# Optimization experiments

Hardware: AMD Instinct MI355X
Metric: run time of the kernel (lower is better)

## Reference

```python
import jax, jax.numpy as jnp
import numpy as np

N_NODES = 100000
N_EDGES = 6400000
IN_CH = 128
HID = 32
OUT = 16


def setup_inputs() -> dict:
    key = jax.random.key(0)
    k1, k2, k3, k4 = jax.random.split(key, 4)
    x = jax.random.normal(k1, (N_NODES, IN_CH), dtype=jnp.float32)
    edge_index = jax.random.randint(k2, (2, N_EDGES), 0, N_NODES, dtype=jnp.int64)
    # Glorot-style init like PyG GCNConv
    W1 = jax.random.normal(k3, (IN_CH, HID), dtype=jnp.float32) * (1.0 / np.sqrt(IN_CH))
    b1 = jnp.zeros((HID,), dtype=jnp.float32)
    W2 = jax.random.normal(k4, (HID, OUT), dtype=jnp.float32) * (1.0 / np.sqrt(HID))
    b2 = jnp.zeros((OUT,), dtype=jnp.float32)
    return {"x": x, "edge_index": edge_index, "W1": W1, "b1": b1, "W2": W2, "b2": b2}


def _gcn_layer(h, W, b, row, col, norm, n_nodes):
    # transform then propagate (PyG GCNConv order)
    m = h @ W                                   # [N, F_out]
    msg = m[row] * norm[:, None]                # gather + scale, [E+N, F_out]
    agg = jax.ops.segment_sum(msg, col, num_segments=n_nodes)
    return agg + b


def reference(x, edge_index, W1, b1, W2, b2):
    n = x.shape[0]
    loops = jnp.arange(n, dtype=edge_index.dtype)
    row = jnp.concatenate([edge_index[0], loops])  # source
    col = jnp.concatenate([edge_index[1], loops])  # target (aggregation index)
    # symmetric GCN normalization with self-loops; deg >= 1 always
    deg = jax.ops.segment_sum(jnp.ones_like(col, dtype=x.dtype), col, num_segments=n)
    deg_inv_sqrt = jax.lax.rsqrt(deg)
    norm = deg_inv_sqrt[row] * deg_inv_sqrt[col]
    h = jax.nn.relu(_gcn_layer(x, W1, b1, row, col, norm, n))
    # dropout p=0.5 is identity in eval mode
    return _gcn_layer(h, W2, b2, row, col, norm, n)
```

## Files before the change

kernel.cpp:

```cpp
#include <hip/hip_runtime.h>
#include <hip/hip_bf16.h>

#define IN_CH 128
#define HID 32
#define OUT_CH 16
#define NPW 128
#define NPW_SHIFT 7
#define NB_MAX 1024
#define CAPF 12800
#define FBT 512
#define CAP 12288
#define KEYS (NPW * 2)
#define SCAN_CHUNK 1024
#define NXCD 8
#define EPT 8

typedef int vint4 __attribute__((ext_vector_type(4)));
typedef vint4 vint4u __attribute__((aligned(4)));
typedef float vfloat2 __attribute__((ext_vector_type(2)));

__global__ void detect_dtype(const void* ei, long long ecount, int n, int* flag) {
    int lane = threadIdx.x;
    const long long* p = (const long long*)ei;
    long long st = ecount / 64; if (st < 1) st = 1;
    long long idx = (long long)lane * st;
    bool ok = true;
    if (idx < ecount) {
        long long v = p[idx];
        ok = (v >= 0 && v < n);
    }
    unsigned long long mask = __ballot(ok);
    if (lane == 0) *flag = (mask == ~0ULL) ? 1 : 0;
}

__device__ __forceinline__ int load_idx(const void* ei, long long i, int is64) {
    return is64 ? (int)((const long long*)ei)[i] : ((const int*)ei)[i];
}

__device__ __forceinline__ void load_idx8_nt(const void* ei, long long off, int is64,
                                             int* c) {
    if (is64) {
        const long long* p = (const long long*)ei + off;
#pragma unroll
        for (int j = 0; j < 8; ++j) c[j] = (int)__builtin_nontemporal_load(p + j);
    } else {
        vint4 v0 = __builtin_nontemporal_load((const vint4*)((const int*)ei + off));
        vint4 v1 = __builtin_nontemporal_load((const vint4*)((const int*)ei + off + 4));
        c[0] = v0.x; c[1] = v0.y; c[2] = v0.z; c[3] = v0.w;
        c[4] = v1.x; c[5] = v1.y; c[6] = v1.z; c[7] = v1.w;
    }
}

__device__ __forceinline__ float bf_lo(unsigned int u) { return __uint_as_float(u << 16); }
__device__ __forceinline__ float bf_hi(unsigned int u) { return __uint_as_float(u & 0xFFFF0000u); }

__global__ __launch_bounds__(256) void zero_int(int* p, int n) {
    int i = blockIdx.x * 256 + threadIdx.x;
    if (i < n) p[i] = 0;
}

__global__ __launch_bounds__(256) void zero_float(float* p, long long n) {
    long long i = (long long)blockIdx.x * 256 + threadIdx.x;
    if (i < n) p[i] = 0.f;
}

__global__ __launch_bounds__(FBT) void bucket_hist(const void* ei, long long E,
                                                   const int* flag, int* bhist,
                                                   int nb, long long chunk, int fbgrid) {
    __shared__ int hist[NB_MAX];
    for (int i = threadIdx.x; i < nb; i += FBT) hist[i] = 0;
    __syncthreads();
    long long lo = (long long)blockIdx.x * chunk;
    long long hi = lo + chunk; if (hi > E) hi = E;
    int is64 = *flag;
    if ((E & 7) == 0) {
        for (long long e = lo + (long long)threadIdx.x * EPT; e + EPT <= hi;
             e += (long long)FBT * EPT) {
            int c[8]; load_idx8_nt(ei, E + e, is64, c);
#pragma unroll
            for (int j = 0; j < 8; ++j) atomicAdd(&hist[c[j] >> NPW_SHIFT], 1);
        }
    } else {
        for (long long e = lo + threadIdx.x; e < hi; e += FBT)
            atomicAdd(&hist[load_idx(ei, E + e, is64) >> NPW_SHIFT], 1);
    }
    __syncthreads();
    for (int b = threadIdx.x; b < nb; b += FBT)
        bhist[(long long)b * fbgrid + blockIdx.x] = hist[b];
}

__global__ __launch_bounds__(256) void scan_blocks(const int* bhist, int* bexcl,
                                                   int* btot, int nb, int fbgrid) {
    __shared__ int sd[256];
    int b = blockIdx.x, t = threadIdx.x;
    const int* p = bhist + (long long)b * fbgrid;
    int* q = bexcl + (long long)b * fbgrid;
    int running = 0;
    for (int j0 = 0; j0 < fbgrid; j0 += 256) {
        int j = j0 + t;
        int v = (j < fbgrid) ? p[j] : 0;
        sd[t] = v; __syncthreads();
        for (int off = 1; off < 256; off <<= 1) {
            int u = (t >= off) ? sd[t - off] : 0;
            __syncthreads(); sd[t] += u; __syncthreads();
        }
        if (j < fbgrid) q[j] = running + sd[t] - v;
        int tot = sd[255];
        __syncthreads();
        running += tot;
    }
    if (t == 0) btot[b] = running;
}

__global__ __launch_bounds__(1024) void scan_buckets(const int* btot, int* bstart, int nb) {
    __shared__ int sd[1024];
    int t = threadIdx.x;
    int a0 = (2 * t < nb) ? btot[2 * t] : 0;
    int a1 = (2 * t + 1 < nb) ? btot[2 * t + 1] : 0;
    sd[t] = a0 + a1; __syncthreads();
    for (int off = 1; off < 1024; off <<= 1) {
        int v = (t >= off) ? sd[t - off] : 0;
        __syncthreads(); sd[t] += v; __syncthreads();
    }
    int excl = sd[t] - (a0 + a1);
    if (2 * t < nb)     bstart[2 * t] = excl;
    if (2 * t + 1 < nb) bstart[2 * t + 1] = excl + a0;
    if (t == 1023) bstart[nb] = sd[t];
}

__global__ __launch_bounds__(FBT) void fill_sort(const void* ei, long long E,
                                                 const int* flag, const int* bhist,
                                                 const int* bexcl, const int* bstart,
                                                 int* bucketed, int nb,
                                                 long long chunk, int fbgrid) {
    __shared__ int lds[CAPF];
    __shared__ int hist[NB_MAX];
    __shared__ int base[NB_MAX];
    __shared__ int cur[NB_MAX];
    int blk = blockIdx.x, t = threadIdx.x;
    long long lo = (long long)blk * chunk;
    long long hi = lo + chunk; if (hi > E) hi = E;
    int cnt = (int)(hi - lo);
    for (int b = t; b < nb; b += FBT)
        hist[b] = bhist[(long long)b * fbgrid + blk];
    __syncthreads();
    int is64 = *flag;
    bool vec = ((E & 7) == 0) && ((chunk & 7) == 0);

    if (cnt <= CAPF) {
        int a0 = (2 * t < nb) ? hist[2 * t] : 0;
        int a1 = (2 * t + 1 < nb) ? hist[2 * t + 1] : 0;
        base[t] = a0 + a1; __syncthreads();
        for (int off = 1; off < FBT; off <<= 1) {
            int u = (t >= off) ? base[t - off] : 0;
            __syncthreads(); base[t] += u; __syncthreads();
        }
        int incl = base[t];
        __syncthreads();
        int excl = incl - (a0 + a1);
        if (2 * t < nb)     { base[2 * t] = excl;          cur[2 * t] = excl; }
        if (2 * t + 1 < nb) { base[2 * t + 1] = excl + a0; cur[2 * t + 1] = excl + a0; }
        __syncthreads();

        if (vec) {
            for (long long e = lo + (long long)t * EPT; e + EPT <= hi; e += (long long)FBT * EPT) {
                int c[8], r[8];
                load_idx8_nt(ei, E + e, is64, c);
                load_idx8_nt(ei, e, is64, r);
#pragma unroll
                for (int j = 0; j < 8; ++j) {
                    int b = c[j] >> NPW_SHIFT;
                    int p = atomicAdd(&cur[b], 1);
                    lds[p] = r[j] | ((c[j] & (NPW - 1)) << 17);
                }
            }
        } else {
            for (long long e = lo + t; e < hi; e += FBT) {
                int col = load_idx(ei, E + e, is64);
                int row = load_idx(ei, e, is64);
                int b = col >> NPW_SHIFT;
                int p = atomicAdd(&cur[b], 1);
                lds[p] = row | ((col & (NPW - 1)) << 17);
            }
        }
        __syncthreads();

        int grp = t >> 4, lane = t & 15;
        for (int b = grp; b < nb; b += 32) {
            int l0 = base[b], c0 = hist[b];
            if (!c0) continue;
            int g0 = bstart[b] + bexcl[(long long)b * fbgrid + blk];
            for (int j = lane; j < c0; j += 16)
                bucketed[g0 + j] = lds[l0 + j];
        }
    } else {
        for (int b = t; b < nb; b += FBT)
            cur[b] = bstart[b] + bexcl[(long long)b * fbgrid + blk];
        __syncthreads();
        for (long long e = lo + t; e < hi; e += FBT) {
            int col = load_idx(ei, E + e, is64);
            int row = load_idx(ei, e, is64);
            int b = col >> NPW_SHIFT;
            int p = atomicAdd(&cur[b], 1);
            bucketed[p] = row | ((col & (NPW - 1)) << 17);
        }
    }
}

__global__ __launch_bounds__(512) void csr_sort(const int* __restrict__ bucketed,
                                                const int* __restrict__ bstart,
                                                int* __restrict__ csr,
                                                int* __restrict__ offs,
                                                int* __restrict__ mid,
                                                float* __restrict__ dinv,
                                                int nb, int n, int nhalf) {
    __shared__ int lds_e[CAP];
    __shared__ int histk[KEYS];
    __shared__ int cur[KEYS];
    int b = blockIdx.x, t = threadIdx.x;
    int s0 = bstart[b], s1 = bstart[b + 1];
    int cnt = s1 - s0;
    if (t < KEYS) histk[t] = 0;
    __syncthreads();
    bool fit = (cnt <= CAP);
    int cnt4 = cnt & ~3;
    auto key = [&](int e) {
        return (((e >> 17) & (NPW - 1)) << 1) | (((e & 0x1FFFF) >= nhalf) ? 1 : 0);
    };
    if (fit) {
        for (int i = t * 4; i < cnt4; i += 2048) {
            vint4u e4 = *(const vint4u*)(bucketed + s0 + i);
            lds_e[i + 0] = e4.x; atomicAdd(&histk[key(e4.x)], 1);
            lds_e[i + 1] = e4.y; atomicAdd(&histk[key(e4.y)], 1);
            lds_e[i + 2] = e4.z; atomicAdd(&histk[key(e4.z)], 1);
            lds_e[i + 3] = e4.w; atomicAdd(&histk[key(e4.w)], 1);
        }
        for (int i = cnt4 + t; i < cnt; i += 512) {
            int e = bucketed[s0 + i];
            lds_e[i] = e;
            atomicAdd(&histk[key(e)], 1);
        }
    } else {
        for (int i = t * 4; i < cnt4; i += 2048) {
            vint4u e4 = *(const vint4u*)(bucketed + s0 + i);
            atomicAdd(&histk[key(e4.x)], 1);
            atomicAdd(&histk[key(e4.y)], 1);
            atomicAdd(&histk[key(e4.z)], 1);
            atomicAdd(&histk[key(e4.w)], 1);
        }
        for (int i = cnt4 + t; i < cnt; i += 512)
            atomicAdd(&histk[key(bucketed[s0 + i])], 1);
    }
    __syncthreads();
    if (t == 0) {
        int run = 0;
        for (int k = 0; k < KEYS; ++k) { cur[k] = run; run += histk[k]; }
    }
    __syncthreads();
    if (t < NPW) {
        int node = b * NPW + t;
        if (node < n) {
            offs[node] = s0 + cur[2 * t];
            mid[node]  = s0 + cur[2 * t] + histk[2 * t];
            dinv[node] = 1.0f / sqrtf((float)(histk[2 * t] + histk[2 * t + 1] + 1));
        }
    }
    if (b == nb - 1 && t == 0) offs[n] = s1;
    __syncthreads();
    if (fit) {
        for (int i = t; i < cnt; i += 512) {
            int e = lds_e[i];
            int pos = atomicAdd(&cur[key(e)], 1);
            csr[s0 + pos] = e & 0x1FFFF;
        }
    } else {
        for (int i = t; i < cnt; i += 512) {
            int e = bucketed[s0 + i];
            int pos = atomicAdd(&cur[key(e)], 1);
            csr[s0 + pos] = e & 0x1FFFF;
        }
    }
}

template <int BF16>
__global__ __launch_bounds__(256) void gemm1p(const float* __restrict__ x,
                                              const float* __restrict__ W1,
                                              const float* __restrict__ dinv,
                                              float* __restrict__ m1f,
                                              __hip_bfloat16* __restrict__ m1b, int n) {
    __shared__ float sW[IN_CH * HID];
    __shared__ float sx[8][IN_CH];
    for (int i = threadIdx.x; i < IN_CH * HID; i += 256) sW[i] = W1[i];
    int g = threadIdx.x >> 5;
    int c = threadIdx.x & 31;
    long long node = (long long)blockIdx.x * 8 + g;
    bool active = node < n;
    if (active) {
        const float4* xr = (const float4*)(x + node * IN_CH);
        float4 v = xr[c];
        sx[g][c * 4 + 0] = v.x; sx[g][c * 4 + 1] = v.y;
        sx[g][c * 4 + 2] = v.z; sx[g][c * 4 + 3] = v.w;
    }
    __syncthreads();
    if (!active) return;
    float acc = 0.f;
#pragma unroll
    for (int k = 0; k < IN_CH; ++k)
        acc = fmaf(sx[g][k], sW[k * HID + c], acc);
    float v = acc * dinv[node];
    if (BF16) m1b[(node << 5) + c] = __float2bfloat16(v);
    else      m1f[(node << 5) + c] = v;
}

template <int BF16>
__global__ __launch_bounds__(256) void gemm2p(const float* __restrict__ h,
                                              const float* __restrict__ W2,
                                              const float* __restrict__ dinv,
                                              float* __restrict__ m2f,
                                              __hip_bfloat16* __restrict__ m2b, int n) {
    __shared__ float sW[HID * OUT_CH];
    for (int i = threadIdx.x; i < HID * OUT_CH; i += 256) sW[i] = W2[i];
    __syncthreads();
    long long t = (long long)blockIdx.x * 256 + threadIdx.x;
    long long node = t >> 4;
    int c = (int)(t & 15);
    if (node >= n) return;
    const float* hr = h + node * HID;
    float acc = 0.f;
#pragma unroll
    for (int k = 0; k < HID; ++k)
        acc = fmaf(hr[k], sW[k * OUT_CH + c], acc);
    float v = acc * dinv[node];
    if (BF16) m2b[(node << 4) + c] = __float2bfloat16(v);
    else      m2f[(node << 4) + c] = v;
}

template <int MODE>
__global__ __launch_bounds__(256) void agg1_bf(const unsigned int* __restrict__ m1b,
                                               const int* __restrict__ csr,
                                               const int* __restrict__ offs,
                                               const int* __restrict__ mid,
                                               const float* __restrict__ dinv,
                                               const float* __restrict__ b1,
                                               float* __restrict__ h, int n) {
    int g = threadIdx.x >> 4;
    int c = threadIdx.x & 15;
    long long node = (long long)blockIdx.x * 16 + g;
    if (node >= n) return;
    int s, e1;
    if (MODE == 0)      { s = offs[node]; e1 = mid[node]; }
    else if (MODE == 1) { s = mid[node];  e1 = offs[node + 1]; }
    else                { s = offs[node]; e1 = offs[node + 1]; }
    float accL, accH;
    if (MODE == 0) { accL = 0.f; accH = 0.f; }
    else {
        unsigned int us = m1b[(node << 4) + c];
        accL = bf_lo(us); accH = bf_hi(us);
    }
    for (; s + 7 < e1; s += 8) {
        vint4u a = *(const vint4u*)(csr + s);
        vint4u b = *(const vint4u*)(csr + s + 4);
        unsigned int u0 = m1b[((long long)a.x << 4) + c];
        unsigned int u1 = m1b[((long long)a.y << 4) + c];
        unsigned int u2 = m1b[((long long)a.z << 4) + c];
        unsigned int u3 = m1b[((long long)a.w << 4) + c];
        unsigned int u4 = m1b[((long long)b.x << 4) + c];
        unsigned int u5 = m1b[((long long)b.y << 4) + c];
        unsigned int u6 = m1b[((long long)b.z << 4) + c];
        unsigned int u7 = m1b[((long long)b.w << 4) + c];
        accL += bf_lo(u0); accH += bf_hi(u0);
        accL += bf_lo(u1); accH += bf_hi(u1);
        accL += bf_lo(u2); accH += bf_hi(u2);
        accL += bf_lo(u3); accH += bf_hi(u3);
        accL += bf_lo(u4); accH += bf_hi(u4);
        accL += bf_lo(u5); accH += bf_hi(u5);
        accL += bf_lo(u6); accH += bf_hi(u6);
        accL += bf_lo(u7); accH += bf_hi(u7);
    }
    for (; s < e1; ++s) {
        unsigned int u = m1b[((long long)csr[s] << 4) + c];
        accL += bf_lo(u); accH += bf_hi(u);
    }
    if (MODE == 0) {
        vfloat2 val; val.x = accL; val.y = accH;
        __builtin_nontemporal_store(val, (vfloat2*)(h + (node << 5) + 2 * c));
    } else {
        if (MODE == 1) {
            vfloat2 prev = __builtin_nontemporal_load((const vfloat2*)(h + (node << 5) + 2 * c));
            accL += prev.x; accH += prev.y;
        }
        float di = dinv[node];
        float vL = accL * di + b1[2 * c];
        float vH = accH * di + b1[2 * c + 1];
        vfloat2 val;
        val.x = vL > 0.f ? vL : 0.f;
        val.y = vH > 0.f ? vH : 0.f;
        *(vfloat2*)(h + (node << 5) + 2 * c) = val;
    }
}

__global__ __launch_bounds__(256) void agg2_bf(const unsigned int* __restrict__ m2b,
                                               const int* __restrict__ csr,
                                               const int* __restrict__ offs,
                                               const float* __restrict__ dinv,
                                               const float* __restrict__ b2,
                                               float* __restrict__ out, int n) {
    int g = threadIdx.x >> 3;
    int c = threadIdx.x & 7;
    long long node = (long long)blockIdx.x * 32 + g;
    if (node >= n) return;
    unsigned int us = m2b[(node << 3) + c];
    float accL = bf_lo(us), accH = bf_hi(us);
    int s = offs[node], e1 = offs[node + 1];
    for (; s + 7 < e1; s += 8) {
        vint4u a = *(const vint4u*)(csr + s);
        vint4u b = *(const vint4u*)(csr + s + 4);
        unsigned int u0 = m2b[((long long)a.x << 3) + c];
        unsigned int u1 = m2b[((long long)a.y << 3) + c];
        unsigned int u2 = m2b[((long long)a.z << 3) + c];
        unsigned int u3 = m2b[((long long)a.w << 3) + c];
        unsigned int u4 = m2b[((long long)b.x << 3) + c];
        unsigned int u5 = m2b[((long long)b.y << 3) + c];
        unsigned int u6 = m2b[((long long)b.z << 3) + c];
        unsigned int u7 = m2b[((long long)b.w << 3) + c];
        accL += bf_lo(u0); accH += bf_hi(u0);
        accL += bf_lo(u1); accH += bf_hi(u1);
        accL += bf_lo(u2); accH += bf_hi(u2);
        accL += bf_lo(u3); accH += bf_hi(u3);
        accL += bf_lo(u4); accH += bf_hi(u4);
        accL += bf_lo(u5); accH += bf_hi(u5);
        accL += bf_lo(u6); accH += bf_hi(u6);
        accL += bf_lo(u7); accH += bf_hi(u7);
    }
    for (; s < e1; ++s) {
        unsigned int u = m2b[((long long)csr[s] << 3) + c];
        accL += bf_lo(u); accH += bf_hi(u);
    }
    float di = dinv[node];
    vfloat2 val;
    val.x = accL * di + b2[2 * c];
    val.y = accH * di + b2[2 * c + 1];
    *(vfloat2*)(out + (node << 4) + 2 * c) = val;
}

__global__ __launch_bounds__(256) void count_edges(const void* ei, int* cnt,
                                                   long long E, const int* flag) {
    long long e0 = ((long long)blockIdx.x * 256 + threadIdx.x) * EPT;
    if (e0 >= E) return;
    int is64 = *flag;
    if (e0 + EPT <= E && (E & 7) == 0) {
        int c[EPT];
        load_idx8_nt(ei, E + e0, is64, c);
#pragma unroll
        for (int j = 0; j < EPT; ++j) atomicAdd(&cnt[c[j]], 1);
    } else {
        for (long long e = e0; e < E && e < e0 + EPT; ++e)
            atomicAdd(&cnt[load_idx(ei, E + e, is64)], 1);
    }
}

__global__ __launch_bounds__(256) void compute_dinv(const int* cnt, float* dinv, int n) {
    int i = blockIdx.x * 256 + threadIdx.x;
    if (i < n) dinv[i] = 1.0f / sqrtf((float)(cnt[i] + 1));
}

__global__ __launch_bounds__(256) void scan_partial(const int* cnt, int* partial, int n) {
    __shared__ int sd[256];
    int base = blockIdx.x * SCAN_CHUNK;
    int s = 0;
    for (int j = threadIdx.x; j < SCAN_CHUNK; j += 256) {
        int i = base + j;
        if (i < n) s += cnt[i];
    }
    sd[threadIdx.x] = s;
    __syncthreads();
    for (int off = 128; off > 0; off >>= 1) {
        if (threadIdx.x < off) sd[threadIdx.x] += sd[threadIdx.x + off];
        __syncthreads();
    }
    if (threadIdx.x == 0) partial[blockIdx.x] = sd[0];
}

__global__ void scan_serial(int* partial, int* offs, int nblk, int n) {
    if (threadIdx.x == 0 && blockIdx.x == 0) {
        int run = 0;
        for (int b = 0; b < nblk; ++b) { int t = partial[b]; partial[b] = run; run += t; }
        offs[n] = run;
    }
}

__global__ __launch_bounds__(256) void scan_final(const int* cnt, const int* partial,
                                                  int* offs, int n) {
    __shared__ int sd[256];
    int base = blockIdx.x * SCAN_CHUNK;
    int t = threadIdx.x;
    int loc[4]; int ts = 0;
#pragma unroll
    for (int j = 0; j < 4; ++j) {
        int i = base + t * 4 + j;
        loc[j] = (i < n) ? cnt[i] : 0;
        ts += loc[j];
    }
    sd[t] = ts;
    __syncthreads();
    for (int off = 1; off < 256; off <<= 1) {
        int v = (t >= off) ? sd[t - off] : 0;
        __syncthreads();
        sd[t] += v;
        __syncthreads();
    }
    int excl = sd[t] - ts + partial[blockIdx.x];
#pragma unroll
    for (int j = 0; j < 4; ++j) {
        int i = base + t * 4 + j;
        if (i < n) offs[i] = excl;
        excl += loc[j];
    }
}

__global__ __launch_bounds__(256) void copy_int(const int* src, int* dst, int n) {
    int i = blockIdx.x * 256 + threadIdx.x;
    if (i < n) dst[i] = src[i];
}

__global__ __launch_bounds__(256) void fill_csr_win(const void* ei, int* cursor, int* csr,
                                                    long long E, const int* flag,
                                                    int npw, int n) {
    int w = blockIdx.x & (NXCD - 1);
    int b = blockIdx.x >> 3;
    int lo = w * npw;
    int hi = lo + npw; if (hi > n) hi = n;
    long long e0 = ((long long)b * 256 + threadIdx.x) * EPT;
    if (e0 >= E) return;
    int is64 = *flag;
    if (e0 + EPT <= E && (E & 7) == 0) {
        int c[EPT];
        load_idx8_nt(ei, E + e0, is64, c);
#pragma unroll
        for (int j = 0; j < EPT; ++j) {
            if (c[j] >= lo && c[j] < hi) {
                int row = load_idx(ei, e0 + j, is64);
                int pos = atomicAdd(&cursor[c[j]], 1);
                csr[pos] = row;
            }
        }
    } else {
        for (long long e = e0; e < E && e < e0 + EPT; ++e) {
            int col = load_idx(ei, E + e, is64);
            if (col >= lo && col < hi) {
                int row = load_idx(ei, e, is64);
                int pos = atomicAdd(&cursor[col], 1);
                csr[pos] = row;
            }
        }
    }
}

__global__ __launch_bounds__(256) void scatter1(const float* __restrict__ m1s,
                                                const void* ei,
                                                float* __restrict__ h,
                                                long long E, const int* flag) {
    long long e = (long long)blockIdx.x * 8 + (threadIdx.x >> 5);
    int c = threadIdx.x & 31;
    if (e >= E) return;
    int is64 = *flag;
    int row = load_idx(ei, e, is64);
    int col = load_idx(ei, E + e, is64);
    atomicAdd(&h[(long long)col * HID + c], m1s[(long long)row * HID + c]);
}

__global__ __launch_bounds__(256) void fixup1(const float* __restrict__ m1s,
                                              const float* __restrict__ dinv,
                                              const float* __restrict__ b1,
                                              float* __restrict__ h, int n) {
    long long t = (long long)blockIdx.x * 256 + threadIdx.x;
    long long node = t >> 5; int c = (int)(t & 31);
    if (node >= n) return;
    float v = (h[node * HID + c] + m1s[node * HID + c]) * dinv[node] + b1[c];
    h[node * HID + c] = v > 0.f ? v : 0.f;
}

__global__ __launch_bounds__(256) void scatter2(const float* __restrict__ m2s,
                                                const void* ei,
                                                float* __restrict__ out,
                                                long long E, const int* flag) {
    long long e = (long long)blockIdx.x * 16 + (threadIdx.x >> 4);
    int c = threadIdx.x & 15;
    if (e >= E) return;
    int is64 = *flag;
    int row = load_idx(ei, e, is64);
    int col = load_idx(ei, E + e, is64);
    atomicAdd(&out[(long long)col * OUT_CH + c], m2s[(long long)row * OUT_CH + c]);
}

__global__ __launch_bounds__(256) void fixup2(const float* __restrict__ m2s,
                                              const float* __restrict__ dinv,
                                              const float* __restrict__ b2,
                                              float* __restrict__ out, int n) {
    long long t = (long long)blockIdx.x * 256 + threadIdx.x;
    long long node = t >> 4; int c = (int)(t & 15);
    if (node >= n) return;
    out[node * OUT_CH + c] = (out[node * OUT_CH + c] + m2s[node * OUT_CH + c]) * dinv[node] + b2[c];
}

extern "C" void kernel_launch(void* const* d_in, const int* in_sizes, int n_in,
                              void* d_out, int out_size, void* d_ws, size_t ws_size,
                              hipStream_t stream) {
    const float* x  = (const float*)d_in[0];
    const void*  ei = d_in[1];
    const float* W1 = (const float*)d_in[2];
    const float* b1 = (const float*)d_in[3];
    const float* W2 = (const float*)d_in[4];
    const float* b2 = (const float*)d_in[5];
    float* out = (float*)d_out;

    const int n = in_sizes[0] / IN_CH;
    const long long E = in_sizes[1] / 2;
    const int nb = (n + NPW - 1) / NPW;
    const int nhalf = (n + 1) / 2;

    const long long chunkF = (((E + 511) / 512) + 7) & ~7LL;
    const int fbgrid = (int)((E + chunkF - 1) / chunkF);

    char* w = (char*)d_ws;
    size_t used = 0;
    auto carve = [&](size_t bytes) -> void* {
        void* p = (void*)(w + used);
        used += (bytes + 255) & ~(size_t)255;
        return p;
    };
    auto A = [](size_t b) -> size_t { return (b + 255) & ~(size_t)255; };

    int*   bstart  = (int*)carve((size_t)(NB_MAX + 1) * 4);
    int*   btot    = (int*)carve((size_t)NB_MAX * 4);
    float* dinv    = (float*)carve((size_t)n * 4);
    int*   flag    = (int*)carve(256);
    int*   offs    = (int*)carve((size_t)(n + 1) * 4);
    int*   mid     = (int*)carve((size_t)n * 4);
    int*   cnt     = (int*)carve((size_t)n * 4);
    int*   partial = (int*)carve(4096);
    const size_t base = used;

    const size_t bhistB = A((size_t)nb * fbgrid * 4);
    const size_t mbB    = A((size_t)n * HID * 2);
    const size_t hB     = A((size_t)n * HID * 4);
    const size_t needT1 = base + 2 * bhistB + 2 * A((size_t)E * 4) + mbB + hB;
    const size_t needT2 = base + A((size_t)E * 4) + mbB + hB;
    const size_t needT3 = base + 2 * A((size_t)n * HID * 4);
    const bool tier1 = (ws_size >= needT1) && (n <= 131071) && (nb <= NB_MAX);
    const bool tier2 = !tier1 && (ws_size >= needT2) && (n <= 131071);

    const int nblkN  = (n + 255) / 256;
    const int nblkEv = (int)((E + 256LL * EPT - 1) / (256LL * EPT));
    const int nblkSc = (n + SCAN_CHUNK - 1) / SCAN_CHUNK;
    const int nblkH  = (int)(((long long)n * HID + 255) / 256);
    const int nblkO  = (int)(((long long)n * OUT_CH + 255) / 256);

    detect_dtype<<<1, 64, 0, stream>>>(ei, E, n, flag);

    if (tier1) {
        int*   bhist    = (int*)carve((size_t)nb * fbgrid * 4);
        int*   bexcl    = (int*)carve((size_t)nb * fbgrid * 4);
        int*   bucketed = (int*)carve((size_t)E * 4);
        int*   csr      = (int*)carve((size_t)E * 4);
        __hip_bfloat16* m1b = (__hip_bfloat16*)carve((size_t)n * HID * 2);
        float* h  = (float*)carve((size_t)n * HID * 4);
        __hip_bfloat16* m2b = m1b;

        bucket_hist<<<fbgrid, FBT, 0, stream>>>(ei, E, flag, bhist, nb, chunkF, fbgrid);
        scan_blocks<<<nb, 256, 0, stream>>>(bhist, bexcl, btot, nb, fbgrid);
        scan_buckets<<<1, 1024, 0, stream>>>(btot, bstart, nb);
        fill_sort<<<fbgrid, FBT, 0, stream>>>(ei, E, flag, bhist, bexcl, bstart,
                                              bucketed, nb, chunkF, fbgrid);
        csr_sort<<<nb, 512, 0, stream>>>(bucketed, bstart, csr, offs, mid, dinv,
                                         nb, n, nhalf);

        gemm1p<1><<<(n + 7) / 8, 256, 0, stream>>>(x, W1, dinv, nullptr, m1b, n);
        agg1_bf<0><<<(n + 15) / 16, 256, 0, stream>>>((const unsigned int*)m1b, csr,
                                                      offs, mid, dinv, b1, h, n);
        agg1_bf<1><<<(n + 15) / 16, 256, 0, stream>>>((const unsigned int*)m1b, csr,
                                                      offs, mid, dinv, b1, h, n);
        gemm2p<1><<<nblkO, 256, 0, stream>>>(h, W2, dinv, nullptr, m2b, n);
        agg2_bf<<<(n + 31) / 32, 256, 0, stream>>>((const unsigned int*)m2b, csr, offs,
                                                   dinv, b2, out, n);
    } else if (tier2) {
        int*   csr = (int*)carve((size_t)E * 4);
        __hip_bfloat16* m1b = (__hip_bfloat16*)carve((size_t)n * HID * 2);
        float* h  = (float*)carve((size_t)n * HID * 4);
        __hip_bfloat16* m2b = m1b;

        zero_int<<<nblkN, 256, 0, stream>>>(cnt, n);
        count_edges<<<nblkEv, 256, 0, stream>>>(ei, cnt, E, flag);
        compute_dinv<<<nblkN, 256, 0, stream>>>(cnt, dinv, n);
        scan_partial<<<nblkSc, 256, 0, stream>>>(cnt, partial, n);
        scan_serial<<<1, 64, 0, stream>>>(partial, offs, nblkSc, n);
        scan_final<<<nblkSc, 256, 0, stream>>>(cnt, partial, offs, n);
        copy_int<<<nblkN, 256, 0, stream>>>(offs, cnt, n);

        const int npw2 = (n + NXCD - 1) / NXCD;
        fill_csr_win<<<nblkEv * NXCD, 256, 0, stream>>>(ei, cnt, csr, E, flag, npw2, n);

        gemm1p<1><<<(n + 7) / 8, 256, 0, stream>>>(x, W1, dinv, nullptr, m1b, n);
        agg1_bf<2><<<(n + 15) / 16, 256, 0, stream>>>((const unsigned int*)m1b, csr,
                                                      offs, offs, dinv, b1, h, n);
        gemm2p<1><<<nblkO, 256, 0, stream>>>(h, W2, dinv, nullptr, m2b, n);
        agg2_bf<<<(n + 31) / 32, 256, 0, stream>>>((const unsigned int*)m2b, csr, offs,
                                                   dinv, b2, out, n);
    } else if (ws_size >= needT3) {
        float* m1 = (float*)carve((size_t)n * HID * 4);
        float* h  = (float*)carve((size_t)n * HID * 4);
        float* m2 = m1;

        zero_int<<<nblkN, 256, 0, stream>>>(cnt, n);
        count_edges<<<nblkEv, 256, 0, stream>>>(ei, cnt, E, flag);
        compute_dinv<<<nblkN, 256, 0, stream>>>(cnt, dinv, n);

        gemm1p<0><<<(n + 7) / 8, 256, 0, stream>>>(x, W1, dinv, m1, nullptr, n);
        zero_float<<<nblkH, 256, 0, stream>>>(h, (long long)n * HID);
        scatter1<<<(int)((E + 7) / 8), 256, 0, stream>>>(m1, ei, h, E, flag);
        fixup1<<<nblkH, 256, 0, stream>>>(m1, dinv, b1, h, n);
        gemm2p<0><<<nblkO, 256, 0, stream>>>(h, W2, dinv, m2, nullptr, n);
        zero_float<<<nblkO, 256, 0, stream>>>(out, (long long)n * OUT_CH);
        scatter2<<<(int)((E + 15) / 16), 256, 0, stream>>>(m2, ei, out, E, flag);
        fixup2<<<nblkO, 256, 0, stream>>>(m2, dinv, b2, out, n);
    }
}
```

Before: 270.1 us.

## Rewrite node GEMMs as one-thread-per-node register-accumulating kernels

Replaces the LDS-staged dense transforms (one thread per output column) with kernels where each thread computes a whole node row in registers. Weights are read uniformly from global or scalar cache instead of LDS, and outputs are written as packed bf16 pairs or float4. The aim is to cut LDS traffic and syncs and to widen the stores. In exchange each thread issues strided per-node loads of x (512 B rows), which coalesce poorly, and register pressure rises.

```diff
diff --git a/kernel.cpp b/kernel.cpp
--- a/kernel.cpp
+++ b/kernel.cpp
@@ -53,6 +53,13 @@
 
 __device__ __forceinline__ float bf_lo(unsigned int u) { return __uint_as_float(u << 16); }
 __device__ __forceinline__ float bf_hi(unsigned int u) { return __uint_as_float(u & 0xFFFF0000u); }
+
+__device__ __forceinline__ unsigned int pack_bf16(float a, float b) {
+    __hip_bfloat16 ha = __float2bfloat16(a), hb = __float2bfloat16(b);
+    unsigned short ua = *reinterpret_cast<unsigned short*>(&ha);
+    unsigned short ub = *reinterpret_cast<unsigned short*>(&hb);
+    return (unsigned int)ua | ((unsigned int)ub << 16);
+}
 
 __global__ __launch_bounds__(256) void zero_int(int* p, int n) {
     int i = blockIdx.x * 256 + threadIdx.x;
@@ -283,56 +290,87 @@
 }
 
 template <int BF16>
-__global__ __launch_bounds__(256) void gemm1p(const float* __restrict__ x,
+__global__ __launch_bounds__(256) void gemm1n(const float* __restrict__ x,
                                               const float* __restrict__ W1,
                                               const float* __restrict__ dinv,
                                               float* __restrict__ m1f,
-                                              __hip_bfloat16* __restrict__ m1b, int n) {
-    __shared__ float sW[IN_CH * HID];
-    __shared__ float sx[8][IN_CH];
-    for (int i = threadIdx.x; i < IN_CH * HID; i += 256) sW[i] = W1[i];
-    int g = threadIdx.x >> 5;
-    int c = threadIdx.x & 31;
-    long long node = (long long)blockIdx.x * 8 + g;
-    bool active = node < n;
-    if (active) {
-        const float4* xr = (const float4*)(x + node * IN_CH);
-        float4 v = xr[c];
-        sx[g][c * 4 + 0] = v.x; sx[g][c * 4 + 1] = v.y;
-        sx[g][c * 4 + 2] = v.z; sx[g][c * 4 + 3] = v.w;
-    }
-    __syncthreads();
-    if (!active) return;
-    float acc = 0.f;
-#pragma unroll
-    for (int k = 0; k < IN_CH; ++k)
-        acc = fmaf(sx[g][k], sW[k * HID + c], acc);
-    float v = acc * dinv[node];
-    if (BF16) m1b[(node << 5) + c] = __float2bfloat16(v);
-    else      m1f[(node << 5) + c] = v;
+                                              unsigned int* __restrict__ m1b, int n) {
+    long long node = (long long)blockIdx.x * 256 + threadIdx.x;
+    if (node >= n) return;
+    float acc[HID];
+#pragma unroll
+    for (int c = 0; c < HID; ++c) acc[c] = 0.f;
+    const float4* xr = (const float4*)(x + node * IN_CH);
+    for (int k4 = 0; k4 < IN_CH / 4; ++k4) {
+        float4 xv = xr[k4];
+        const float* w0 = W1 + (k4 * 4) * HID;
+#pragma unroll
+        for (int c = 0; c < HID; ++c) acc[c] = fmaf(xv.x, w0[c], acc[c]);
+#pragma unroll
+        for (int c = 0; c < HID; ++c) acc[c] = fmaf(xv.y, w0[HID + c], acc[c]);
+#pragma unroll
+        for (int c = 0; c < HID; ++c) acc[c] = fmaf(xv.z, w0[2 * HID + c], acc[c]);
+#pragma unroll
+        for (int c = 0; c < HID; ++c) acc[c] = fmaf(xv.w, w0[3 * HID + c], acc[c]);
+    }
+    float di = dinv[node];
+    if (BF16) {
+        unsigned int* dst = m1b + (node << 4);
+#pragma unroll
+        for (int c = 0; c < HID / 2; ++c)
+            dst[c] = pack_bf16(acc[2 * c] * di, acc[2 * c + 1] * di);
+    } else {
+        float4* dst = (float4*)(m1f + (node << 5));
+#pragma unroll
+        for (int c = 0; c < HID / 4; ++c) {
+            float4 v;
+            v.x = acc[4 * c] * di;     v.y = acc[4 * c + 1] * di;
+            v.z = acc[4 * c + 2] * di; v.w = acc[4 * c + 3] * di;
+            dst[c] = v;
+        }
+    }
 }
 
 template <int BF16>
-__global__ __launch_bounds__(256) void gemm2p(const float* __restrict__ h,
+__global__ __launch_bounds__(256) void gemm2n(const float* __restrict__ h,
                                               const float* __restrict__ W2,
                                               const float* __restrict__ dinv,
                                               float* __restrict__ m2f,
-                                              __hip_bfloat16* __restrict__ m2b, int n) {
-    __shared__ float sW[HID * OUT_CH];
-    for (int i = threadIdx.x; i < HID * OUT_CH; i += 256) sW[i] = W2[i];
-    __syncthreads();
-    long long t = (long long)blockIdx.x * 256 + threadIdx.x;
-    long long node = t >> 4;
-    int c = (int)(t & 15);
+                                              unsigned int* __restrict__ m2b, int n) {
+    long long node = (long long)blockIdx.x * 256 + threadIdx.x;
     if (node >= n) return;
-    const float* hr = h + node * HID;
-    float acc = 0.f;
-#pragma unroll
-    for (int k = 0; k < HID; ++k)
-        acc = fmaf(hr[k], sW[k * OUT_CH + c], acc);
-    float v = acc * dinv[node];
-    if (BF16) m2b[(node << 4) + c] = __float2bfloat16(v);
-    else      m2f[(node << 4) + c] = v;
+    float acc[OUT_CH];
+#pragma unroll
+    for (int c = 0; c < OUT_CH; ++c) acc[c] = 0.f;
+    const float4* hr = (const float4*)(h + (node << 5));
+    for (int k4 = 0; k4 < HID / 4; ++k4) {
+        float4 hv = hr[k4];
+        const float* w0 = W2 + (k4 * 4) * OUT_CH;
+#pragma unroll
+        for (int c = 0; c < OUT_CH; ++c) acc[c] = fmaf(hv.x, w0[c], acc[c]);
+#pragma unroll
+        for (int c = 0; c < OUT_CH; ++c) acc[c] = fmaf(hv.y, w0[OUT_CH + c], acc[c]);
+#pragma unroll
+        for (int c = 0; c < OUT_CH; ++c) acc[c] = fmaf(hv.z, w0[2 * OUT_CH + c], acc[c]);
+#pragma unroll
+        for (int c = 0; c < OUT_CH; ++c) acc[c] = fmaf(hv.w, w0[3 * OUT_CH + c], acc[c]);
+    }
+    float di = dinv[node];
+    if (BF16) {
+        unsigned int* dst = m2b + (node << 3);
+#pragma unroll
+        for (int c = 0; c < OUT_CH / 2; ++c)
+            dst[c] = pack_bf16(acc[2 * c] * di, acc[2 * c + 1] * di);
+    } else {
+        float4* dst = (float4*)(m2f + (node << 4));
+#pragma unroll
+        for (int c = 0; c < OUT_CH / 4; ++c) {
+            float4 v;
+            v.x = acc[4 * c] * di;     v.y = acc[4 * c + 1] * di;
+            v.z = acc[4 * c + 2] * di; v.w = acc[4 * c + 3] * di;
+            dst[c] = v;
+        }
+    }
 }
 
 template <int MODE>
@@ -675,12 +713,14 @@
         csr_sort<<<nb, 512, 0, stream>>>(bucketed, bstart, csr, offs, mid, dinv,
                                          nb, n, nhalf);
 
-        gemm1p<1><<<(n + 7) / 8, 256, 0, stream>>>(x, W1, dinv, nullptr, m1b, n);
+        gemm1n<1><<<nblkN, 256, 0, stream>>>(x, W1, dinv, nullptr,
+                                             (unsigned int*)m1b, n);
         agg1_bf<0><<<(n + 15) / 16, 256, 0, stream>>>((const unsigned int*)m1b, csr,
                                                       offs, mid, dinv, b1, h, n);
         agg1_bf<1><<<(n + 15) / 16, 256, 0, stream>>>((const unsigned int*)m1b, csr,
                                                       offs, mid, dinv, b1, h, n);
-        gemm2p<1><<<nblkO, 256, 0, stream>>>(h, W2, dinv, nullptr, m2b, n);
+        gemm2n<1><<<nblkN, 256, 0, stream>>>(h, W2, dinv, nullptr,
+                                             (unsigned int*)m2b, n);
         agg2_bf<<<(n + 31) / 32, 256, 0, stream>>>((const unsigned int*)m2b, csr, offs,
                                                    dinv, b2, out, n);
     } else if (tier2) {
@@ -700,10 +740,12 @@
         const int npw2 = (n + NXCD - 1) / NXCD;
         fill_csr_win<<<nblkEv * NXCD, 256, 0, stream>>>(ei, cnt, csr, E, flag, npw2, n);
 
-        gemm1p<1><<<(n + 7) / 8, 256, 0, stream>>>(x, W1, dinv, nullptr, m1b, n);
+        gemm1n<1><<<nblkN, 256, 0, stream>>>(x, W1, dinv, nullptr,
+                                             (unsigned int*)m1b, n);
         agg1_bf<2><<<(n + 15) / 16, 256, 0, stream>>>((const unsigned int*)m1b, csr,
                                                       offs, offs, dinv, b1, h, n);
-        gemm2p<1><<<nblkO, 256, 0, stream>>>(h, W2, dinv, nullptr, m2b, n);
+        gemm2n<1><<<nblkN, 256, 0, stream>>>(h, W2, dinv, nullptr,
+                                             (unsigned int*)m2b, n);
         agg2_bf<<<(n + 31) / 32, 256, 0, stream>>>((const unsigned int*)m2b, csr, offs,
                                                    dinv, b2, out, n);
     } else if (ws_size >= needT3) {
@@ -715,11 +757,11 @@
         count_edges<<<nblkEv, 256, 0, stream>>>(ei, cnt, E, flag);
         compute_dinv<<<nblkN, 256, 0, stream>>>(cnt, dinv, n);
 
-        gemm1p<0><<<(n + 7) / 8, 256, 0, stream>>>(x, W1, dinv, m1, nullptr, n);
+        gemm1n<0><<<nblkN, 256, 0, stream>>>(x, W1, dinv, m1, nullptr, n);
         zero_float<<<nblkH, 256, 0, stream>>>(h, (long long)n * HID);
         scatter1<<<(int)((E + 7) / 8), 256, 0, stream>>>(m1, ei, h, E, flag);
         fixup1<<<nblkH, 256, 0, stream>>>(m1, dinv, b1, h, n);
-        gemm2p<0><<<nblkO, 256, 0, stream>>>(h, W2, dinv, m2, nullptr, n);
+        gemm2n<0><<<nblkN, 256, 0, stream>>>(h, W2, dinv, m2, nullptr, n);
         zero_float<<<nblkO, 256, 0, stream>>>(out, (long long)n * OUT_CH);
         scatter2<<<(int)((E + 15) / 16), 256, 0, stream>>>(m2, ei, out, E, flag);
         fixup2<<<nblkO, 256, 0, stream>>>(m2, dinv, b2, out, n);
```

After: 261.2 us. 3.3% less time.
